# Kernel tuning notes

Hardware: AMD Instinct MI355X
Metric: run time of the kernel (lower is better)

## Reference

```python
import jax, jax.numpy as jnp
import numpy as np

N_EMBD = 768
N_EXPERTS = 8
TOP_K = 2
D_FF = 4 * N_EMBD


def setup_inputs() -> dict:
    key = jax.random.key(0)
    k1, k2, k3, k4 = jax.random.split(key, 4)
    x = jax.random.normal(k1, (2, 2048, N_EMBD), dtype=jnp.float32)
    gate_w = jax.random.normal(k2, (N_EMBD, N_EXPERTS), dtype=jnp.float32) * (1.0 / np.sqrt(N_EMBD))
    w_fc = jax.random.normal(k3, (N_EXPERTS, N_EMBD, D_FF), dtype=jnp.float32) * (1.0 / np.sqrt(N_EMBD))
    w_proj = jax.random.normal(k4, (N_EXPERTS, D_FF, N_EMBD), dtype=jnp.float32) * (1.0 / np.sqrt(D_FF))
    return {"x": x, "gate_w": gate_w, "w_fc": w_fc, "w_proj": w_proj}


def reference(x, gate_w, w_fc, w_proj):
    B, S, D = x.shape
    E = w_fc.shape[0]
    xt = x.reshape(-1, D)                    # [T, D]
    T = xt.shape[0]
    scores = xt @ gate_w                      # [T, E]
    expert_weights, expert_indices = jax.lax.top_k(scores, TOP_K)  # [T, K]
    expert_weights = jax.nn.softmax(expert_weights, axis=-1)
    # per-token combine weight for each expert (0 if expert not selected)
    comb = jnp.zeros((T, E), dtype=xt.dtype)
    comb = comb.at[jnp.arange(T)[:, None], expert_indices].add(expert_weights)  # [T, E]
    out = jnp.zeros_like(xt)
    for e in range(E):  # fixed small loop over experts
        h = jax.nn.gelu(xt @ w_fc[e], approximate=False)  # torch nn.GELU default = exact erf
        y_e = h @ w_proj[e]                               # [T, D]
        out = out + comb[:, e:e + 1] * y_e
    return out.reshape(B, S, D)
```

## Files before the change

kernel.cpp:

```cpp
#include <hip/hip_runtime.h>
#include <hip/hip_bf16.h>
#include <math.h>

#define T_TOK 4096
#define D_EMB 768
#define DFF   3072
#define N_EXP 8
#define MAXT  72
#define CNTS  16

typedef __attribute__((ext_vector_type(8))) short bf16x8;
typedef __attribute__((ext_vector_type(4))) float f32x4;

typedef __attribute__((address_space(3))) unsigned int lds_u32_t;
typedef __attribute__((address_space(1))) unsigned int glob_u32_t;

__device__ __forceinline__ void gload16(const void* g, void* l) {
  __builtin_amdgcn_global_load_lds((const glob_u32_t*)g, (lds_u32_t*)l, 16, 0, 0);
}

__device__ __forceinline__ short f2bf(float f) {
  union { __hip_bfloat16 b; short s; } u;
  u.b = __float2bfloat16(f);
  return u.s;
}

__device__ __forceinline__ float gelu_f(float v) {
  float u = 0.7978845608f * v * (1.0f + 0.044715f * v * v);
  float a = fabsf(u);
  float em = __expf(-2.0f * a);
  float th = (1.0f - em) / (1.0f + em);
  th = (u < 0.0f) ? -th : th;
  return 0.5f * v * (1.0f + th);
}

__device__ __forceinline__ int swz(int row) { return (row ^ (row >> 2)) & 3; }

__global__ void zero_init_kernel(float4* __restrict__ out4, int n4, int* __restrict__ cnt) {
  int i = blockIdx.x * blockDim.x + threadIdx.x;
  if (i < N_EXP * CNTS) cnt[i] = 0;
  float4 z; z.x = z.y = z.z = z.w = 0.f;
  for (int j = i; j < n4; j += gridDim.x * blockDim.x) out4[j] = z;
}

__global__ __launch_bounds__(256)
void slab_weights(const float* __restrict__ src, short* __restrict__ dst,
                  int Kt, int Nt, int NCT, int NKTall) {
  __shared__ float t32[32][132];
  int ct = blockIdx.x, kt = blockIdx.y, e = blockIdx.z;
  const float* s = src + ((size_t)e * Kt + kt * 32) * Nt + ct * 128;
  int tid = threadIdx.x;
#pragma unroll
  for (int p4 = 0; p4 < 4; p4++) {
    int idx = tid + p4 * 256;
    int kl = idx >> 5, c4 = idx & 31;
    float4 v = *(const float4*)&s[(size_t)kl * Nt + c4 * 4];
    t32[kl][c4 * 4 + 0] = v.x; t32[kl][c4 * 4 + 1] = v.y;
    t32[kl][c4 * 4 + 2] = v.z; t32[kl][c4 * 4 + 3] = v.w;
  }
  __syncthreads();
  short* d = dst + (((size_t)e * NCT + ct) * NKTall + kt) * 4096;
#pragma unroll
  for (int i = 0; i < 2; i++) {
    int seg = tid + i * 256;
    int row = seg >> 2, p = seg & 3;
    int q = p ^ swz(row);
    union { short sv[8]; uint4 u; } o;
#pragma unroll
    for (int j = 0; j < 8; j++) o.sv[j] = f2bf(t32[q * 8 + j][row]);
    *(uint4*)&d[(size_t)seg * 8] = o.u;
  }
}

__global__ __launch_bounds__(256)
void gate_kernel(const float* __restrict__ x, const float* __restrict__ gw,
                 int* __restrict__ cnt, int* __restrict__ tok,
                 float* __restrict__ wgt) {
  __shared__ int lcnt[N_EXP];
  __shared__ int gbase[N_EXP];
  __shared__ int le[32];
  __shared__ float lw[32];
  __shared__ int lpos[32];
  int tid = threadIdx.x, lane = tid & 63, wid = tid >> 6;
  if (tid < N_EXP) lcnt[tid] = 0;
  __syncthreads();

#pragma unroll
  for (int i = 0; i < 4; i++) {
    int t = blockIdx.x * 16 + wid * 4 + i;
    float s[N_EXP];
#pragma unroll
    for (int e = 0; e < N_EXP; e++) s[e] = 0.f;
#pragma unroll
    for (int dd = 0; dd < D_EMB / 64; dd++) {
      int d = dd * 64 + lane;
      float xv = x[(size_t)t * D_EMB + d];
#pragma unroll
      for (int e = 0; e < N_EXP; e++) s[e] += xv * gw[d * N_EXP + e];
    }
#pragma unroll
    for (int e = 0; e < N_EXP; e++) {
#pragma unroll
      for (int off = 32; off > 0; off >>= 1) s[e] += __shfl_xor(s[e], off, 64);
    }
    if (lane == 0) {
      int e0 = 0;
#pragma unroll
      for (int e = 1; e < N_EXP; e++) if (s[e] > s[e0]) e0 = e;
      int e1 = -1;
#pragma unroll
      for (int e = 0; e < N_EXP; e++) {
        if (e == e0) continue;
        if (e1 < 0 || s[e] > s[e1]) e1 = e;
      }
      float p1 = __expf(s[e1] - s[e0]);
      float inv = 1.f / (1.f + p1);
      int idx = (wid * 4 + i) * 2;
      le[idx] = e0; lw[idx] = inv;           lpos[idx] = atomicAdd(&lcnt[e0], 1);
      le[idx + 1] = e1; lw[idx + 1] = p1 * inv; lpos[idx + 1] = atomicAdd(&lcnt[e1], 1);
    }
  }
  __syncthreads();
  if (tid < N_EXP) gbase[tid] = atomicAdd(&cnt[tid * CNTS], lcnt[tid]);
  __syncthreads();
  if (tid < 32) {
    int e = le[tid];
    int t = blockIdx.x * 16 + (tid >> 1);
    int p = gbase[e] + lpos[tid];
    tok[e * T_TOK + p] = t;
    wgt[e * T_TOK + p] = lw[tid];
  }
}

__global__ void plan_kernel(const int* __restrict__ cnt, int* __restrict__ offs,
                            int* __restrict__ tile_e, int* __restrict__ tile_rt,
                            int* __restrict__ ntiles) {
  if (threadIdx.x != 0 || blockIdx.x != 0) return;
  int o = 0, nt = 0;
  for (int e = 0; e < N_EXP; e++) {
    offs[e] = o;
    int tc = (cnt[e * CNTS] + 127) >> 7;
    for (int i = 0; i < tc; i++) { tile_e[nt] = e; tile_rt[nt] = i; nt++; }
    o += cnt[e * CNTS];
  }
  *ntiles = nt;
}

__global__ __launch_bounds__(256)
void gatherA_kernel(const float* __restrict__ x, const int* __restrict__ tok,
                    const int* __restrict__ cnt, const int* __restrict__ offs,
                    const int* __restrict__ tile_e, const int* __restrict__ tile_rt,
                    const int* __restrict__ ntiles, short* __restrict__ aslab) {
  int tile = blockIdx.x, kt = blockIdx.y;
  if (tile >= *ntiles) return;
  int e = tile_e[tile], rt = tile_rt[tile];
  int ne = cnt[e * CNTS];
  int tid = threadIdx.x;
  short* d = aslab + ((size_t)tile * 24 + kt) * 4096;
#pragma unroll
  for (int i = 0; i < 2; i++) {
    int seg = tid + i * 256;
    int row = seg >> 2, p = seg & 3;
    int q = p ^ swz(row);
    int r = rt * 128 + row; if (r >= ne) r = ne - 1;
    int t = tok[e * T_TOK + r];
    const float* src = x + (size_t)t * D_EMB + kt * 32 + q * 8;
    union { short sv[8]; uint4 u; } o;
#pragma unroll
    for (int j = 0; j < 8; j++) o.sv[j] = f2bf(src[j]);
    *(uint4*)&d[(size_t)seg * 8] = o.u;
  }
}

template<int KDIM, int NDIM, int SPLITK, int GRT, int GCT, int EPI>
__global__ __launch_bounds__(256, 4)
void moe_gemm(const short* __restrict__ Aop, const short* __restrict__ Bslab,
              const int* __restrict__ tok, const float* __restrict__ wgt,
              const int* __restrict__ cnt, const int* __restrict__ offs,
              const int* __restrict__ tile_e, const int* __restrict__ tile_rt,
              const int* __restrict__ ntiles,
              short* __restrict__ hout, float* __restrict__ fout) {
  const int COLT = NDIM / 128;
  const int KS = KDIM / SPLITK;
  const int NKT = KS / 32;
  const int NKTALL = KDIM / 32;
  const int BPS = GRT * GCT;
  const int NCG = COLT / GCT;
  const int PER_SK = MAXT * COLT;

  int nwg = gridDim.x;
  int cpx = nwg >> 3;
  int logical = (blockIdx.x & 7) * cpx + (blockIdx.x >> 3);
  int sk = logical / PER_SK;
  int rem = logical % PER_SK;
  int super = rem / BPS, inner = rem % BPS;
  int band = super / NCG, cg = super % NCG;
  int tile = band * GRT + (inner % GRT);
  int ct = cg * GCT + (inner / GRT);
  if (tile >= *ntiles) return;
  int e = tile_e[tile], rt = tile_rt[tile];
  int ne = cnt[e * CNTS];
  int base = offs[e];

  __shared__ __align__(16) short As[2][128 * 32];
  __shared__ __align__(16) short Bs[2][128 * 32];

  int tid = threadIdx.x;
  int lane = tid & 63;
  int wid = tid >> 6;

  const int AKT = (EPI == 0) ? 4096 : 32;
  const short* aptr[2];
  const short* bptr[2];
  int lofs[2];
#pragma unroll
  for (int i = 0; i < 2; i++) {
    int seg = tid + i * 256;
    int row = seg >> 2, p = seg & 3;
    int q = p ^ swz(row);
    if (EPI == 0) {
      aptr[i] = Aop + ((size_t)tile * 24) * 4096 + seg * 8;
    } else {
      int r = rt * 128 + row; if (r >= ne) r = ne - 1;
      aptr[i] = Aop + (size_t)(base + r) * KDIM + sk * KS + q * 8;
    }
    bptr[i] = Bslab + (((size_t)e * COLT + ct) * NKTALL + sk * NKT) * 4096 + seg * 8;
    lofs[i] = seg * 8;
  }

  f32x4 acc[4][4];
#pragma unroll
  for (int m = 0; m < 4; m++)
#pragma unroll
    for (int n = 0; n < 4; n++) acc[m][n] = (f32x4){0.f, 0.f, 0.f, 0.f};

  int wr = (wid >> 1) * 64, wc = (wid & 1) * 64;

#pragma unroll
  for (int i = 0; i < 2; i++) {
    gload16(aptr[i], &As[0][lofs[i]]);
    gload16(bptr[i], &Bs[0][lofs[i]]);
  }
  __syncthreads();

  int cur = 0;
  for (int kt = 0; kt < NKT; ++kt) {
    if (kt + 1 < NKT) {
#pragma unroll
      for (int i = 0; i < 2; i++) {
        gload16(aptr[i] + (size_t)(kt + 1) * AKT, &As[cur ^ 1][lofs[i]]);
        gload16(bptr[i] + (size_t)(kt + 1) * 4096, &Bs[cur ^ 1][lofs[i]]);
      }
    }
    int cb = lane >> 4;
    bf16x8 af[4], bv[4];
#pragma unroll
    for (int m = 0; m < 4; m++) {
      int row = wr + m * 16 + (lane & 15);
      af[m] = *(const bf16x8*)&As[cur][row * 32 + ((cb ^ swz(row)) * 8)];
    }
#pragma unroll
    for (int n = 0; n < 4; n++) {
      int row = wc + n * 16 + (lane & 15);
      bv[n] = *(const bf16x8*)&Bs[cur][row * 32 + ((cb ^ swz(row)) * 8)];
    }
#pragma unroll
    for (int m = 0; m < 4; m++)
#pragma unroll
      for (int n = 0; n < 4; n++)
        acc[m][n] = __builtin_amdgcn_mfma_f32_16x16x32_bf16(af[m], bv[n], acc[m][n], 0, 0, 0);
    __syncthreads();
    cur ^= 1;
  }

  int colbase = ct * 128 + wc;
#pragma unroll
  for (int m = 0; m < 4; m++) {
#pragma unroll
    for (int j = 0; j < 4; j++) {
      int rloc = rt * 128 + wr + m * 16 + ((lane >> 4) << 2) + j;
      if (rloc < ne) {
        if (EPI == 0) {
          size_t hrow = (size_t)(base + rloc) * NDIM;
#pragma unroll
          for (int n = 0; n < 4; n++)
            hout[hrow + colbase + n * 16 + (lane & 15)] = f2bf(gelu_f(acc[m][n][j]));
        } else {
          int t = tok[e * T_TOK + rloc];
          float w = wgt[e * T_TOK + rloc];
          float* orow = fout + (size_t)t * NDIM + colbase + (lane & 15);
#pragma unroll
          for (int n = 0; n < 4; n++)
            atomicAdd(orow + n * 16, w * acc[m][n][j]);
        }
      }
    }
  }
}

extern "C" void kernel_launch(void* const* d_in, const int* in_sizes, int n_in,
                              void* d_out, int out_size, void* d_ws, size_t ws_size,
                              hipStream_t stream) {
  const float* x   = (const float*)d_in[0];
  const float* gw  = (const float*)d_in[1];
  const float* wfc = (const float*)d_in[2];
  const float* wpj = (const float*)d_in[3];
  float* out = (float*)d_out;

  char* ws = (char*)d_ws;
  const size_t SZ_ASLAB = (size_t)MAXT * 24 * 4096 * 2;
  const size_t SZ_BFC   = (size_t)N_EXP * 24 * 24 * 4096 * 2;
  const size_t SZ_BPJ   = (size_t)N_EXP * 6 * 96 * 4096 * 2;
  const size_t SZ_H     = (size_t)2 * T_TOK * DFF * 2;
  short* aslab = (short*)(ws);
  short* bfc   = (short*)(ws + SZ_ASLAB);
  short* bpj   = (short*)(ws + SZ_ASLAB + SZ_BFC);
  short* h     = (short*)(ws + SZ_ASLAB + SZ_BFC + SZ_BPJ);
  char* p2     = ws + SZ_ASLAB + SZ_BFC + SZ_BPJ + SZ_H;
  int*   tok  = (int*)(p2);
  float* wgt  = (float*)(p2 + (size_t)N_EXP * T_TOK * 4);
  char* p3    = p2 + (size_t)N_EXP * T_TOK * 8;
  int*   cnt     = (int*)(p3);
  int*   offs    = (int*)(p3 + 1024);
  int*   tile_e  = (int*)(p3 + 1024 + 64);
  int*   tile_rt = (int*)(p3 + 1024 + 64 + 512);
  int*   ntiles  = (int*)(p3 + 1024 + 64 + 1024);

  int n4 = out_size / 4;
  zero_init_kernel<<<2048, 256, 0, stream>>>((float4*)out, n4, cnt);
  slab_weights<<<dim3(24, 24, N_EXP), 256, 0, stream>>>(wfc, bfc, D_EMB, DFF, 24, 24);
  slab_weights<<<dim3(6, 96, N_EXP), 256, 0, stream>>>(wpj, bpj, DFF, D_EMB, 6, 96);
  gate_kernel<<<T_TOK / 16, 256, 0, stream>>>(x, gw, cnt, tok, wgt);
  plan_kernel<<<1, 1, 0, stream>>>(cnt, offs, tile_e, tile_rt, ntiles);
  gatherA_kernel<<<dim3(MAXT, 24), 256, 0, stream>>>(x, tok, cnt, offs, tile_e, tile_rt, ntiles, aslab);
  moe_gemm<D_EMB, DFF, 1, 8, 8, 0><<<MAXT * (DFF / 128), 256, 0, stream>>>(
      aslab, bfc, tok, wgt, cnt, offs, tile_e, tile_rt, ntiles, h, nullptr);
  moe_gemm<DFF, D_EMB, 2, 8, 6, 1><<<2 * MAXT * (D_EMB / 128), 256, 0, stream>>>(
      h, bpj, tok, wgt, cnt, offs, tile_e, tile_rt, ntiles, nullptr, out);
}
```

Baseline: 219.9 us.

## Warp-specialize expert GEMMs with producer waves and a 4-stage LDS ring

Replaces the double-buffered global_load_lds GEMM with a warp-specialized design. Four producer waves load A/B tiles through registers into a 4-slot LDS ring, and four consumer waves run the MFMAs, with the two sides synchronised by LDS counter flags and spin-waits. The aim is to overlap global loads with MFMA work and to remove the block-wide barrier on every k-step. In exchange it doubles the block size, spends extra LDS and registers on staging, and adds spin-wait and atomic-flag overhead that could lower occupancy.

```diff
diff --git a/kernel.cpp b/kernel.cpp
--- a/kernel.cpp
+++ b/kernel.cpp
@@ -11,13 +11,6 @@
 
 typedef __attribute__((ext_vector_type(8))) short bf16x8;
 typedef __attribute__((ext_vector_type(4))) float f32x4;
-
-typedef __attribute__((address_space(3))) unsigned int lds_u32_t;
-typedef __attribute__((address_space(1))) unsigned int glob_u32_t;
-
-__device__ __forceinline__ void gload16(const void* g, void* l) {
-  __builtin_amdgcn_global_load_lds((const glob_u32_t*)g, (lds_u32_t*)l, 16, 0, 0);
-}
 
 __device__ __forceinline__ short f2bf(float f) {
   union { __hip_bfloat16 b; short s; } u;
@@ -35,6 +28,13 @@
 }
 
 __device__ __forceinline__ int swz(int row) { return (row ^ (row >> 2)) & 3; }
+
+__device__ __forceinline__ void spin_ge(const int* f, int tgt) {
+  volatile const int* vf = f;
+  while (*vf < tgt) { asm volatile("s_sleep 1"); }
+  __builtin_amdgcn_sched_barrier(0);
+  asm volatile("" ::: "memory");
+}
 
 __global__ void zero_init_kernel(float4* __restrict__ out4, int n4, int* __restrict__ cnt) {
   int i = blockIdx.x * blockDim.x + threadIdx.x;
@@ -173,23 +173,24 @@
 }
 
 template<int KDIM, int NDIM, int SPLITK, int GRT, int GCT, int EPI>
-__global__ __launch_bounds__(256, 4)
-void moe_gemm(const short* __restrict__ Aop, const short* __restrict__ Bslab,
-              const int* __restrict__ tok, const float* __restrict__ wgt,
-              const int* __restrict__ cnt, const int* __restrict__ offs,
-              const int* __restrict__ tile_e, const int* __restrict__ tile_rt,
-              const int* __restrict__ ntiles,
-              short* __restrict__ hout, float* __restrict__ fout) {
+__global__ __launch_bounds__(512, 4)
+void pc_gemm(const short* __restrict__ Aop, const short* __restrict__ Bslab,
+             const int* __restrict__ tok, const float* __restrict__ wgt,
+             const int* __restrict__ cnt, const int* __restrict__ offs,
+             const int* __restrict__ tile_e, const int* __restrict__ tile_rt,
+             const int* __restrict__ ntiles,
+             short* __restrict__ hout, float* __restrict__ fout) {
   const int COLT = NDIM / 128;
   const int KS = KDIM / SPLITK;
   const int NKT = KS / 32;
   const int NKTALL = KDIM / 32;
+  const int ASTRIDE = (EPI == 0) ? 4096 : 32;
   const int BPS = GRT * GCT;
   const int NCG = COLT / GCT;
   const int PER_SK = MAXT * COLT;
-
-  int nwg = gridDim.x;
-  int cpx = nwg >> 3;
+  static_assert(NKT % 4 == 0 && NKT >= 8, "ring needs NKT%4==0");
+
+  int nwg = gridDim.x, cpx = nwg >> 3;
   int logical = (blockIdx.x & 7) * cpx + (blockIdx.x >> 3);
   int sk = logical / PER_SK;
   int rem = logical % PER_SK;
@@ -202,99 +203,146 @@
   int ne = cnt[e * CNTS];
   int base = offs[e];
 
-  __shared__ __align__(16) short As[2][128 * 32];
-  __shared__ __align__(16) short Bs[2][128 * 32];
-
-  int tid = threadIdx.x;
-  int lane = tid & 63;
-  int wid = tid >> 6;
-
-  const int AKT = (EPI == 0) ? 4096 : 32;
-  const short* aptr[2];
-  const short* bptr[2];
-  int lofs[2];
-#pragma unroll
-  for (int i = 0; i < 2; i++) {
-    int seg = tid + i * 256;
-    int row = seg >> 2, p = seg & 3;
-    int q = p ^ swz(row);
-    if (EPI == 0) {
-      aptr[i] = Aop + ((size_t)tile * 24) * 4096 + seg * 8;
-    } else {
-      int r = rt * 128 + row; if (r >= ne) r = ne - 1;
-      aptr[i] = Aop + (size_t)(base + r) * KDIM + sk * KS + q * 8;
-    }
-    bptr[i] = Bslab + (((size_t)e * COLT + ct) * NKTALL + sk * NKT) * 4096 + seg * 8;
-    lofs[i] = seg * 8;
-  }
-
-  f32x4 acc[4][4];
-#pragma unroll
-  for (int m = 0; m < 4; m++)
-#pragma unroll
-    for (int n = 0; n < 4; n++) acc[m][n] = (f32x4){0.f, 0.f, 0.f, 0.f};
-
-  int wr = (wid >> 1) * 64, wc = (wid & 1) * 64;
-
-#pragma unroll
-  for (int i = 0; i < 2; i++) {
-    gload16(aptr[i], &As[0][lofs[i]]);
-    gload16(bptr[i], &Bs[0][lofs[i]]);
-  }
-  __syncthreads();
-
-  int cur = 0;
-  for (int kt = 0; kt < NKT; ++kt) {
-    if (kt + 1 < NKT) {
-#pragma unroll
-      for (int i = 0; i < 2; i++) {
-        gload16(aptr[i] + (size_t)(kt + 1) * AKT, &As[cur ^ 1][lofs[i]]);
-        gload16(bptr[i] + (size_t)(kt + 1) * 4096, &Bs[cur ^ 1][lofs[i]]);
-      }
-    }
+  __shared__ __align__(16) short AsR[4][4096];
+  __shared__ __align__(16) short BsR[4][4096];
+  __shared__ int prodf[4];
+  __shared__ int consf[4];
+
+  int tid = threadIdx.x, lane = tid & 63, wid = tid >> 6;
+  if (tid < 4) { prodf[tid] = 0; consf[tid] = 0; }
+  __syncthreads();
+
+  if (wid < 4) {
+    int wr = (wid >> 1) * 64, wc = (wid & 1) * 64;
     int cb = lane >> 4;
-    bf16x8 af[4], bv[4];
+    int offa[4], offb[4];
 #pragma unroll
     for (int m = 0; m < 4; m++) {
       int row = wr + m * 16 + (lane & 15);
-      af[m] = *(const bf16x8*)&As[cur][row * 32 + ((cb ^ swz(row)) * 8)];
+      offa[m] = row * 32 + ((cb ^ swz(row)) * 8);
     }
 #pragma unroll
     for (int n = 0; n < 4; n++) {
       int row = wc + n * 16 + (lane & 15);
-      bv[n] = *(const bf16x8*)&Bs[cur][row * 32 + ((cb ^ swz(row)) * 8)];
-    }
+      offb[n] = row * 32 + ((cb ^ swz(row)) * 8);
+    }
+
+    f32x4 acc[4][4];
 #pragma unroll
     for (int m = 0; m < 4; m++)
 #pragma unroll
-      for (int n = 0; n < 4; n++)
-        acc[m][n] = __builtin_amdgcn_mfma_f32_16x16x32_bf16(af[m], bv[n], acc[m][n], 0, 0, 0);
-    __syncthreads();
-    cur ^= 1;
-  }
-
-  int colbase = ct * 128 + wc;
-#pragma unroll
-  for (int m = 0; m < 4; m++) {
-#pragma unroll
-    for (int j = 0; j < 4; j++) {
-      int rloc = rt * 128 + wr + m * 16 + ((lane >> 4) << 2) + j;
-      if (rloc < ne) {
-        if (EPI == 0) {
-          size_t hrow = (size_t)(base + rloc) * NDIM;
+      for (int n = 0; n < 4; n++) acc[m][n] = (f32x4){0.f, 0.f, 0.f, 0.f};
+
+#pragma unroll 1
+    for (int tg = 0; tg < NKT / 4; ++tg) {
+      int tgt = 4 * (tg + 1);
+#pragma unroll
+      for (int b = 0; b < 4; ++b) {
+        spin_ge(&prodf[b], tgt);
+        bf16x8 af[4], bv[4];
+#pragma unroll
+        for (int m = 0; m < 4; m++) af[m] = *(const bf16x8*)&AsR[b][offa[m]];
+#pragma unroll
+        for (int n = 0; n < 4; n++) bv[n] = *(const bf16x8*)&BsR[b][offb[n]];
+        asm volatile("s_waitcnt lgkmcnt(0)" ::: "memory");
+        __builtin_amdgcn_sched_barrier(0);
+        if (lane == 0) atomicAdd(&consf[b], 1);
+#pragma unroll
+        for (int m = 0; m < 4; m++)
 #pragma unroll
           for (int n = 0; n < 4; n++)
-            hout[hrow + colbase + n * 16 + (lane & 15)] = f2bf(gelu_f(acc[m][n][j]));
-        } else {
-          int t = tok[e * T_TOK + rloc];
-          float w = wgt[e * T_TOK + rloc];
-          float* orow = fout + (size_t)t * NDIM + colbase + (lane & 15);
-#pragma unroll
-          for (int n = 0; n < 4; n++)
-            atomicAdd(orow + n * 16, w * acc[m][n][j]);
+            acc[m][n] = __builtin_amdgcn_mfma_f32_16x16x32_bf16(
+                af[m], bv[n], acc[m][n], 0, 0, 0);
+      }
+    }
+
+    int colbase = ct * 128 + wc;
+#pragma unroll
+    for (int m = 0; m < 4; m++) {
+#pragma unroll
+      for (int j = 0; j < 4; j++) {
+        int rloc = rt * 128 + wr + m * 16 + ((lane >> 4) << 2) + j;
+        if (rloc < ne) {
+          if (EPI == 0) {
+            size_t hrow = (size_t)(base + rloc) * NDIM;
+#pragma unroll
+            for (int n = 0; n < 4; n++)
+              hout[hrow + colbase + n * 16 + (lane & 15)] = f2bf(gelu_f(acc[m][n][j]));
+          } else {
+            int t = tok[e * T_TOK + rloc];
+            float w = wgt[e * T_TOK + rloc];
+            float* orow = fout + (size_t)t * NDIM + colbase + (lane & 15);
+#pragma unroll
+            for (int n = 0; n < 4; n++)
+              atomicAdd(orow + n * 16, w * acc[m][n][j]);
+          }
         }
       }
     }
+  } else {
+    int pl = tid - 256;
+    const short* ap0;
+    const short* ap1;
+    if (EPI == 0) {
+      ap0 = Aop + (size_t)tile * NKTALL * 4096 + pl * 8;
+      ap1 = ap0 + 2048;
+    } else {
+      {
+        int seg = pl;
+        int row = seg >> 2, p = seg & 3;
+        int q = p ^ swz(row);
+        int r = rt * 128 + row; if (r >= ne) r = ne - 1;
+        ap0 = Aop + (size_t)(base + r) * KDIM + sk * KS + q * 8;
+      }
+      {
+        int seg = pl + 256;
+        int row = seg >> 2, p = seg & 3;
+        int q = p ^ swz(row);
+        int r = rt * 128 + row; if (r >= ne) r = ne - 1;
+        ap1 = Aop + (size_t)(base + r) * KDIM + sk * KS + q * 8;
+      }
+    }
+    const short* bp0 = Bslab + (((size_t)e * COLT + ct) * NKTALL + sk * NKT) * 4096 + pl * 8;
+    const short* bp1 = bp0 + 2048;
+    int lo0 = pl * 8, lo1 = (pl + 256) * 8;
+
+    f32x4 s0a0, s0a1, s0b0, s0b1;
+    f32x4 s1a0, s1a1, s1b0, s1b1;
+
+#define LOADP(A0, A1, B0, B1, KT) do {                                        \
+    int kc_ = (KT) < NKT ? (KT) : (NKT - 1);                                  \
+    A0 = *(const f32x4*)(ap0 + (size_t)kc_ * ASTRIDE);                        \
+    A1 = *(const f32x4*)(ap1 + (size_t)kc_ * ASTRIDE);                        \
+    B0 = *(const f32x4*)(bp0 + (size_t)kc_ * 4096);                          \
+    B1 = *(const f32x4*)(bp1 + (size_t)kc_ * 4096);                          \
+  } while (0)
+#define PUTP(A0, A1, B0, B1, B) do {                                          \
+    *(f32x4*)&AsR[B][lo0] = A0; *(f32x4*)&AsR[B][lo1] = A1;                   \
+    *(f32x4*)&BsR[B][lo0] = B0; *(f32x4*)&BsR[B][lo1] = B1;                   \
+    asm volatile("s_waitcnt lgkmcnt(0)" ::: "memory");                        \
+    __builtin_amdgcn_sched_barrier(0);                                        \
+    if (lane == 0) atomicAdd(&prodf[B], 1);                                   \
+  } while (0)
+
+    LOADP(s0a0, s0a1, s0b0, s0b1, 0);
+#pragma unroll 1
+    for (int tg = 0; tg < NKT / 4; ++tg) {
+      int ctgt = 4 * tg;
+      LOADP(s1a0, s1a1, s1b0, s1b1, 4 * tg + 1);
+      spin_ge(&consf[0], ctgt);
+      PUTP(s0a0, s0a1, s0b0, s0b1, 0);
+      LOADP(s0a0, s0a1, s0b0, s0b1, 4 * tg + 2);
+      spin_ge(&consf[1], ctgt);
+      PUTP(s1a0, s1a1, s1b0, s1b1, 1);
+      LOADP(s1a0, s1a1, s1b0, s1b1, 4 * tg + 3);
+      spin_ge(&consf[2], ctgt);
+      PUTP(s0a0, s0a1, s0b0, s0b1, 2);
+      LOADP(s0a0, s0a1, s0b0, s0b1, 4 * tg + 4);
+      spin_ge(&consf[3], ctgt);
+      PUTP(s1a0, s1a1, s1b0, s1b1, 3);
+    }
+#undef PUTP
+#undef LOADP
   }
 }
 
@@ -333,8 +381,8 @@
   gate_kernel<<<T_TOK / 16, 256, 0, stream>>>(x, gw, cnt, tok, wgt);
   plan_kernel<<<1, 1, 0, stream>>>(cnt, offs, tile_e, tile_rt, ntiles);
   gatherA_kernel<<<dim3(MAXT, 24), 256, 0, stream>>>(x, tok, cnt, offs, tile_e, tile_rt, ntiles, aslab);
-  moe_gemm<D_EMB, DFF, 1, 8, 8, 0><<<MAXT * (DFF / 128), 256, 0, stream>>>(
+  pc_gemm<D_EMB, DFF, 1, 8, 8, 0><<<MAXT * (DFF / 128), 512, 0, stream>>>(
       aslab, bfc, tok, wgt, cnt, offs, tile_e, tile_rt, ntiles, h, nullptr);
-  moe_gemm<DFF, D_EMB, 2, 8, 6, 1><<<2 * MAXT * (D_EMB / 128), 256, 0, stream>>>(
+  pc_gemm<DFF, D_EMB, 2, 8, 6, 1><<<2 * MAXT * (D_EMB / 128), 512, 0, stream>>>(
       h, bpj, tok, wgt, cnt, offs, tile_e, tile_rt, ntiles, nullptr, out);
 }
```

Result: slower. 256.0 us (+16.4%).
